# Kernel tuning notes

Hardware: AMD Instinct MI355X
Metric: run time of the kernel (lower is better)

Reference implementation:

```python
import jax, jax.numpy as jnp
import numpy as np

N_NODES = 100000
N_EDGES = 1200000
NFEAT, NHID, NCLASS = 64, 256, 40
DROP_RATE = 0.5
ORDER = 8


def setup_inputs() -> dict:
    key = jax.random.key(0)
    k = jax.random.split(key, 6)
    x = jax.random.normal(k[0], (N_NODES, NFEAT), dtype=jnp.float32)
    edge_index = jax.random.randint(k[1], (2, N_EDGES), 0, N_NODES, dtype=jnp.int64)
    stdv1 = 1.0 / np.sqrt(NHID)
    stdv2 = 1.0 / np.sqrt(NCLASS)
    W1 = jax.random.normal(k[2], (NFEAT, NHID), dtype=jnp.float32) * stdv1
    b1 = jax.random.normal(k[3], (NHID,), dtype=jnp.float32) * stdv1
    W2 = jax.random.normal(k[4], (NHID, NCLASS), dtype=jnp.float32) * stdv2
    b2 = jax.random.normal(k[5], (NCLASS,), dtype=jnp.float32) * stdv2
    return {"x": x, "edge_index": edge_index, "W1": W1, "b1": b1, "W2": W2, "b2": b2}


def _norm_adj(edge_index, n):
    # A + I, then D^{-1/2} (A+I) D^{-1/2}  (GCN symmetric normalization)
    loops = jnp.arange(n, dtype=edge_index.dtype)
    row = jnp.concatenate([edge_index[0], loops])
    col = jnp.concatenate([edge_index[1], loops])
    ones = jnp.ones(row.shape[0], dtype=jnp.float32)
    deg = jax.ops.segment_sum(ones, row, num_segments=n)  # row sums (self-loops guarantee deg>=1)
    d_inv_sqrt = 1.0 / jnp.sqrt(deg)
    ew = d_inv_sqrt[row] * d_inv_sqrt[col]  # [E+N] edge weights
    return row, col, ew


def reference(x, edge_index, W1, b1, W2, b2):
    n = x.shape[0]
    row, col, ew = _norm_adj(edge_index, n)

    def spmm(h):  # out[row] += ew * h[col]
        return jax.ops.segment_sum(ew[:, None] * h[col], row, num_segments=n)

    # eval-mode input scaling (training=False branch of GRAND.forward)
    h = x * (1.0 - DROP_RATE)
    y = h
    for _ in range(ORDER):
        h = spmm(h)
        y = y + h
    y = y / (ORDER + 1.0)

    # MLP in eval mode: dropouts are no-ops, use_bn=False
    hid = jax.nn.relu(y @ W1 + b1)
    return hid @ W2 + b2
```

## Files before the change

kernel.cpp:

```cpp
#include <hip/hip_runtime.h>

#define NN 100000
#define NE 1200000
#define NF 64
#define NH 256
#define NC 40
#define ORDER_C 8
#define SC 1024
#define BINB 1024
#define BCAP 165000
#define CCAP (NE + 7 * NN)

typedef __attribute__((ext_vector_type(8))) short short8;
typedef __attribute__((ext_vector_type(4))) float f32x4;

__device__ __forceinline__ unsigned bf16r(float x) {
    unsigned u = __float_as_uint(x);
    return (u + 0x7FFFu + ((u >> 16) & 1u)) >> 16;
}
__device__ __forceinline__ unsigned packbf(float lo, float hi) {
    return bf16r(lo) | (bf16r(hi) << 16);
}
__device__ __forceinline__ float bflo(unsigned u) { return __uint_as_float(u << 16); }
__device__ __forceinline__ float bfhi(unsigned u) { return __uint_as_float(u & 0xFFFF0000u); }


static __global__ __launch_bounds__(256) void k_bin(const int* __restrict__ rows,
                                                    const int* __restrict__ cols,
                                                    int* __restrict__ bcnt,
                                                    int* __restrict__ browb,
                                                    int* __restrict__ bcolb, int E)
{
    __shared__ int rbuf[BINB];
    __shared__ unsigned short lofs[BINB];
    __shared__ int hist[8], basew[8];
    int t = threadIdx.x;
    int e0 = blockIdx.x * BINB;
    int m = E - e0; if (m > BINB) m = BINB;
    if (t < 8) hist[t] = 0;
    __syncthreads();
    for (int i = t; i < m; i += 256) {
        int r = rows[e0 + i];
        rbuf[i] = r;
        int b = r / 12500;
        lofs[i] = (unsigned short)atomicAdd(&hist[b], 1);
    }
    __syncthreads();
    if (t < 8) basew[t] = atomicAdd(&bcnt[t], hist[t]);
    __syncthreads();
    for (int i = t; i < m; i += 256) {
        int r = rbuf[i];
        int b = r / 12500;
        size_t pos = (size_t)b * BCAP + basew[b] + lofs[i];
        browb[pos] = r;
        bcolb[pos] = cols[e0 + i];
    }
}


static __global__ __launch_bounds__(256) void k_cnt2(const int* __restrict__ browb,
                                                     const int* __restrict__ bcnt,
                                                     int* __restrict__ cnt)
{
    int grp = blockIdx.x & 7;
    int m = bcnt[grp];
    const int* src = browb + (size_t)grp * BCAP;
    int stride = (gridDim.x >> 3) * 256;
    for (int i = (blockIdx.x >> 3) * 256 + threadIdx.x; i < m; i += stride)
        atomicAdd(&cnt[src[i]], 1);
}


static __global__ __launch_bounds__(256) void k_bsum(const int* __restrict__ cnt,
                                                     int* __restrict__ bsum, int n)
{
    __shared__ int red[256];
    int t = threadIdx.x;
    int idx = blockIdx.x * SC + t * 4;
    int s = 0;
    if (idx + 3 < n) {
        int4 q = *(const int4*)&cnt[idx];
        s = ((q.x + 7) & ~7) + ((q.y + 7) & ~7) + ((q.z + 7) & ~7) + ((q.w + 7) & ~7);
    } else {
        for (int j = 0; j < 4; ++j) if (idx + j < n) s += (cnt[idx + j] + 7) & ~7;
    }
    red[t] = s;
    __syncthreads();
    for (int off = 128; off > 0; off >>= 1) {
        if (t < off) red[t] += red[t + off];
        __syncthreads();
    }
    if (t == 0) bsum[blockIdx.x] = red[0];
}

static __global__ __launch_bounds__(128) void k_scanb(const int* __restrict__ bsum,
                                                      int* __restrict__ boff,
                                                      int* __restrict__ rp, int nb, int n)
{
    __shared__ int red[128];
    int t = threadIdx.x;
    int v = (t < nb) ? bsum[t] : 0;
    red[t] = v;
    __syncthreads();
    for (int off = 1; off < 128; off <<= 1) {
        int x = (t >= off) ? red[t - off] : 0;
        __syncthreads();
        red[t] += x;
        __syncthreads();
    }
    if (t < nb) boff[t] = (t == 0) ? 0 : red[t - 1];
    if (t == 0) rp[n] = red[127];
}

static __global__ __launch_bounds__(256) void k_scan3(const int* __restrict__ cnt,
                                                      const int* __restrict__ boff,
                                                      int* __restrict__ rp,
                                                      float2* __restrict__ drd, int n)
{
    __shared__ int red[256];
    int t = threadIdx.x;
    int idx = blockIdx.x * SC + t * 4;
    int v[4] = {0, 0, 0, 0};
    if (idx + 3 < n) {
        int4 q = *(const int4*)&cnt[idx];
        v[0] = q.x; v[1] = q.y; v[2] = q.z; v[3] = q.w;
    } else {
        for (int j = 0; j < 4; ++j) if (idx + j < n) v[j] = cnt[idx + j];
    }
    int p[4];
    #pragma unroll
    for (int j = 0; j < 4; ++j) p[j] = (v[j] + 7) & ~7;
    red[t] = p[0] + p[1] + p[2] + p[3];
    __syncthreads();
    for (int off = 1; off < 256; off <<= 1) {
        int x = (t >= off) ? red[t - off] : 0;
        __syncthreads();
        red[t] += x;
        __syncthreads();
    }
    int run = ((t == 0) ? 0 : red[t - 1]) + boff[blockIdx.x];
    #pragma unroll
    for (int j = 0; j < 4; ++j) {
        if (idx + j < n) {
            rp[idx + j] = run;
            float d1 = rsqrtf((float)(v[j] + 1));
            drd[idx + j] = make_float2(d1, (float)(v[j] + 1) * d1);
            run += p[j];
        }
    }
}


static __global__ __launch_bounds__(256) void k_fillc(int4* __restrict__ ccol4, int cap4, int val)
{
    int i = blockIdx.x * 256 + threadIdx.x;
    if (i < cap4) ccol4[i] = make_int4(val, val, val, val);
}


static __global__ __launch_bounds__(256) void k_scat2(const int* __restrict__ browb,
                                                      const int* __restrict__ bcolb,
                                                      const int* __restrict__ bcnt,
                                                      int* __restrict__ fillpos,
                                                      int* __restrict__ ccol)
{
    int grp = blockIdx.x & 7;
    int m = bcnt[grp];
    const int* srcr = browb + (size_t)grp * BCAP;
    const int* srcc = bcolb + (size_t)grp * BCAP;
    int stride = (gridDim.x >> 3) * 256;
    for (int i = (blockIdx.x >> 3) * 256 + threadIdx.x; i < m; i += stride) {
        int r = srcr[i];
        int pos = atomicAdd(&fillpos[r], 1);
        ccol[pos] = srcc[i];
    }
}


static __global__ __launch_bounds__(256) void k_pack(const float* __restrict__ W1,
                                                     const float* __restrict__ W2,
                                                     unsigned short* __restrict__ w1f,
                                                     unsigned short* __restrict__ w2f)
{
    int t = blockIdx.x * 256 + threadIdx.x;
    if (t < 2048) {
        int lane = t & 63;
        int g = lane >> 4, col = (lane & 15) + ((t >> 6) & 15) * 16;
        int s = t >> 10;
        unsigned short* p = w1f + (size_t)t * 8;
        #pragma unroll
        for (int e = 0; e < 8; ++e) {
            int k = 32 * s + 8 * g + e;
            p[e] = (unsigned short)bf16r(W1[k * NH + col]);
        }
    } else if (t < 2048 + 1536) {
        int u = t - 2048;
        int lane = u & 63;
        int tile = u >> 6;
        int nt = tile % 3, s = tile / 3;
        int g = lane >> 4, col = (lane & 15) + nt * 16;
        unsigned short* p = w2f + (size_t)u * 8;
        #pragma unroll
        for (int e = 0; e < 8; ++e) {
            int k = 32 * s + 8 * g + e;
            p[e] = (col < NC) ? (unsigned short)bf16r(W2[k * NC + col]) : 0;
        }
    }
}


static __global__ __launch_bounds__(256) void k_init(const float4* __restrict__ x4,
                                                     float4* __restrict__ y4,
                                                     uint4* __restrict__ ga,
                                                     uint4* __restrict__ gbp,
                                                     const float2* __restrict__ drd,
                                                     int nchunk)
{
    int i = blockIdx.x * 256 + threadIdx.x;
    if (i >= nchunk) {
        if (i < nchunk + 8) {
            uint4 z = make_uint4(0, 0, 0, 0);
            ga[i] = z; gbp[i] = z;
        }
        return;
    }
    float d1 = drd[i >> 3].x;
    float4 a = x4[i * 2], b = x4[i * 2 + 1];
    a.x *= 0.5f; a.y *= 0.5f; a.z *= 0.5f; a.w *= 0.5f;
    b.x *= 0.5f; b.y *= 0.5f; b.z *= 0.5f; b.w *= 0.5f;
    y4[i * 2] = a; y4[i * 2 + 1] = b;
    ga[i] = make_uint4(packbf(a.x * d1, a.y * d1), packbf(a.z * d1, a.w * d1),
                       packbf(b.x * d1, b.y * d1), packbf(b.z * d1, b.w * d1));
}


template<bool ACC>
static __global__ __launch_bounds__(256) void k_spmm(const uint2* __restrict__ gb,
                                                     uint2* __restrict__ go,
                                                     float4* __restrict__ y4,
                                                     const int* __restrict__ rp,
                                                     const int* __restrict__ ccol,
                                                     const float2* __restrict__ drd, int n)
{
    int wid  = (blockIdx.x * 256 + threadIdx.x) >> 6;
    int lane = threadIdx.x & 63;
    int row  = wid * 4 + (lane >> 4);
    int j    = lane & 15;
    if (row >= n) return;
    int s = rp[row], e = rp[row + 1];

    float a0 = 0.f, a1 = 0.f, a2 = 0.f, a3 = 0.f;
    float b0 = 0.f, b1 = 0.f, b2 = 0.f, b3 = 0.f;
    for (int i = s; i < e; i += 8) {
        int4 cA = *(const int4*)&ccol[i];
        int4 cB = *(const int4*)&ccol[i + 4];
        uint2 h0 = gb[(size_t)cA.x * 16 + j];
        uint2 h1 = gb[(size_t)cA.y * 16 + j];
        uint2 h2 = gb[(size_t)cA.z * 16 + j];
        uint2 h3 = gb[(size_t)cA.w * 16 + j];
        uint2 h4 = gb[(size_t)cB.x * 16 + j];
        uint2 h5 = gb[(size_t)cB.y * 16 + j];
        uint2 h6 = gb[(size_t)cB.z * 16 + j];
        uint2 h7 = gb[(size_t)cB.w * 16 + j];
        a0 += bflo(h0.x); a1 += bfhi(h0.x); a2 += bflo(h0.y); a3 += bfhi(h0.y);
        b0 += bflo(h1.x); b1 += bfhi(h1.x); b2 += bflo(h1.y); b3 += bfhi(h1.y);
        a0 += bflo(h2.x); a1 += bfhi(h2.x); a2 += bflo(h2.y); a3 += bfhi(h2.y);
        b0 += bflo(h3.x); b1 += bfhi(h3.x); b2 += bflo(h3.y); b3 += bfhi(h3.y);
        a0 += bflo(h4.x); a1 += bfhi(h4.x); a2 += bflo(h4.y); a3 += bfhi(h4.y);
        b0 += bflo(h5.x); b1 += bfhi(h5.x); b2 += bflo(h5.y); b3 += bfhi(h5.y);
        a0 += bflo(h6.x); a1 += bfhi(h6.x); a2 += bflo(h6.y); a3 += bfhi(h6.y);
        b0 += bflo(h7.x); b1 += bfhi(h7.x); b2 += bflo(h7.y); b3 += bfhi(h7.y);
    }

    float2 dr = drd[row];
    uint2 gs = gb[(size_t)row * 16 + j];
    float g0 = bflo(gs.x), g1 = bfhi(gs.x), g2 = bflo(gs.y), g3 = bfhi(gs.y);
    float s0 = (a0 + b0) + g0;
    float s1 = (a1 + b1) + g1;
    float s2 = (a2 + b2) + g2;
    float s3 = (a3 + b3) + g3;
    float h0 = dr.x * s0, h1 = dr.x * s1, h2 = dr.x * s2, h3 = dr.x * s3;
    go[(size_t)row * 16 + j] = make_uint2(packbf(dr.x * h0, dr.x * h1),
                                          packbf(dr.x * h2, dr.x * h3));
    if (ACC) {
        float4 yv = y4[(size_t)row * 16 + j];
        yv.x += fmaf(g0, dr.y, h0);
        yv.y += fmaf(g1, dr.y, h1);
        yv.z += fmaf(g2, dr.y, h2);
        yv.w += fmaf(g3, dr.y, h3);
        y4[(size_t)row * 16 + j] = yv;
    }
}


#define YSTR 72
#define HSTR 264

static __global__ __launch_bounds__(256) void k_mlp(const float4* __restrict__ y4,
                                                    const short8* __restrict__ w1f,
                                                    const short8* __restrict__ w2f,
                                                    const float* __restrict__ b1,
                                                    const float* __restrict__ b2,
                                                    float* __restrict__ out, int n)
{
    __shared__ short lds[64 * HSTR];
    int t = threadIdx.x;
    int lane = t & 63;
    int w = t >> 6;
    int base = blockIdx.x * 64;
    const float S = 1.f / 9.f;

    {
        int r = t >> 2, q = t & 3;
        int row = base + r;
        unsigned v[8];
        if (row < n) {
            const float4* yp = y4 + (size_t)row * 16 + q * 4;
            #pragma unroll
            for (int i = 0; i < 4; ++i) {
                float4 f = yp[i];
                v[i * 2]     = packbf(f.x * S, f.y * S);
                v[i * 2 + 1] = packbf(f.z * S, f.w * S);
            }
        } else {
            #pragma unroll
            for (int i = 0; i < 8; ++i) v[i] = 0;
        }
        uint4* dst = (uint4*)&lds[r * YSTR + q * 16];
        dst[0] = make_uint4(v[0], v[1], v[2], v[3]);
        dst[1] = make_uint4(v[4], v[5], v[6], v[7]);
    }
    __syncthreads();

    int m = lane & 15, g = lane >> 4;

    f32x4 acc[4][4];
    {
        short8 a[4][2];
        #pragma unroll
        for (int mt = 0; mt < 4; ++mt)
            #pragma unroll
            for (int s = 0; s < 2; ++s)
                a[mt][s] = *(const short8*)&lds[(mt * 16 + m) * YSTR + s * 32 + g * 8];
        #pragma unroll
        for (int nt4 = 0; nt4 < 4; ++nt4) {
            int nt = w * 4 + nt4;
            short8 b0  = w1f[nt * 64 + lane];
            short8 b1v = w1f[(16 + nt) * 64 + lane];
            float bias = b1[nt * 16 + m];
            #pragma unroll
            for (int mt = 0; mt < 4; ++mt) {
                f32x4 c = {bias, bias, bias, bias};
                c = __builtin_amdgcn_mfma_f32_16x16x32_bf16(a[mt][0], b0,  c, 0, 0, 0);
                c = __builtin_amdgcn_mfma_f32_16x16x32_bf16(a[mt][1], b1v, c, 0, 0, 0);
                acc[mt][nt4] = c;
            }
        }
    }
    __syncthreads();

    {
        #pragma unroll
        for (int mt = 0; mt < 4; ++mt)
            #pragma unroll
            for (int nt4 = 0; nt4 < 4; ++nt4) {
                int col = w * 64 + nt4 * 16 + m;
                #pragma unroll
                for (int r = 0; r < 4; ++r) {
                    float hv = fmaxf(acc[mt][nt4][r], 0.f);
                    lds[(mt * 16 + g * 4 + r) * HSTR + col] = (short)bf16r(hv);
                }
            }
    }
    __syncthreads();

    {
        short8 a2[8];
        #pragma unroll
        for (int s = 0; s < 8; ++s)
            a2[s] = *(const short8*)&lds[(w * 16 + m) * HSTR + s * 32 + g * 8];
        #pragma unroll
        for (int nt = 0; nt < 3; ++nt) {
            int col = nt * 16 + m;
            float bias = (col < NC) ? b2[col] : 0.f;
            f32x4 c = {bias, bias, bias, bias};
            #pragma unroll
            for (int s = 0; s < 8; ++s)
                c = __builtin_amdgcn_mfma_f32_16x16x32_bf16(a2[s], w2f[(s * 3 + nt) * 64 + lane], c, 0, 0, 0);
            if (col < NC) {
                #pragma unroll
                for (int r = 0; r < 4; ++r) {
                    int row = base + w * 16 + g * 4 + r;
                    if (row < n) out[(size_t)row * NC + col] = c[r];
                }
            }
        }
    }
}


extern "C" void kernel_launch(void* const* d_in, const int* in_sizes, int n_in,
                              void* d_out, int out_size, void* d_ws, size_t ws_size,
                              hipStream_t stream)
{
    const float* x  = (const float*)d_in[0];
    const int*   ei = (const int*)d_in[1];
    const float* W1 = (const float*)d_in[2];
    const float* b1 = (const float*)d_in[3];
    const float* W2 = (const float*)d_in[4];
    const float* b2 = (const float*)d_in[5];
    float* out = (float*)d_out;

    const int n = NN, E = NE;
    const int nb = (n + SC - 1) / SC;

    char* ws = (char*)d_ws;
    size_t off = 0;
    auto alloc = [&](size_t bytes) -> void* {
        void* p = ws + off;
        off = (off + bytes + 255) & ~(size_t)255;
        return p;
    };
    int*    cnt   = (int*)   alloc((size_t)n * 4);
    int*    fill  = (int*)   alloc((size_t)n * 4);
    int*    rp    = (int*)   alloc((size_t)(n + 1) * 4);
    float2* drd   = (float2*)alloc((size_t)n * 8);
    int*    bsum  = (int*)   alloc(128 * 4);
    int*    boff  = (int*)   alloc(128 * 4);
    int*    bcnt  = (int*)   alloc(8 * 4);
    int*    browb = (int*)   alloc((size_t)8 * BCAP * 4);
    int*    bcolb = (int*)   alloc((size_t)8 * BCAP * 4);
    int*    ccol  = (int*)   alloc((size_t)CCAP * 4);
    unsigned short* w1f = (unsigned short*)alloc(2048 * 8 * 2);
    unsigned short* w2f = (unsigned short*)alloc(1536 * 8 * 2);
    uint4* ha   = (uint4*)alloc((size_t)(n + 1) * NF * 2);
    uint4* hbuf = (uint4*)alloc((size_t)(n + 1) * NF * 2);
    float* y    = (float*)alloc((size_t)n * NF * 4);

    hipMemsetAsync(cnt, 0, (size_t)n * 4, stream);
    hipMemsetAsync(bcnt, 0, 8 * 4, stream);

    const int* rows = ei;
    const int* cols = ei + E;

    k_bin   <<<(E + BINB - 1) / BINB, 256, 0, stream>>>(rows, cols, bcnt, browb, bcolb, E);
    k_cnt2  <<<4096, 256, 0, stream>>>(browb, bcnt, cnt);
    k_bsum  <<<nb, 256, 0, stream>>>(cnt, bsum, n);
    k_scanb <<<1, 128, 0, stream>>>(bsum, boff, rp, nb, n);
    k_scan3 <<<nb, 256, 0, stream>>>(cnt, boff, rp, drd, n);
    hipMemcpyAsync(fill, rp, (size_t)n * 4, hipMemcpyDeviceToDevice, stream);
    k_fillc <<<(CCAP / 4 + 255) / 256, 256, 0, stream>>>((int4*)ccol, CCAP / 4, n);
    k_scat2 <<<4096, 256, 0, stream>>>(browb, bcolb, bcnt, fill, ccol);
    k_pack  <<<14, 256, 0, stream>>>(W1, W2, w1f, w2f);

    int nchunk = n * 8;
    k_init<<<(nchunk + 8 + 255) / 256, 256, 0, stream>>>((const float4*)x, (float4*)y,
                                                         ha, hbuf, drd, nchunk);

    uint4* cur = ha;
    uint4* nxt = hbuf;
    int spmm_blocks = (n + 15) / 16;
    for (int it = 0; it < ORDER_C; ++it) {
        if (it & 1)
            k_spmm<true><<<spmm_blocks, 256, 0, stream>>>((const uint2*)cur, (uint2*)nxt,
                                                          (float4*)y, rp, ccol, drd, n);
        else
            k_spmm<false><<<spmm_blocks, 256, 0, stream>>>((const uint2*)cur, (uint2*)nxt,
                                                           (float4*)y, rp, ccol, drd, n);
        uint4* tswap = cur; cur = nxt; nxt = tswap;
    }

    k_mlp<<<(n + 63) / 64, 256, 0, stream>>>((const float4*)y, (const short8*)w1f,
                                             (const short8*)w2f, b1, b2, out, n);
}
```

Baseline: 405.9 us.

## Use XCD-aware dynamic chunk claiming for CSR build and drop fill pass

The count and scatter kernels now read the XCC id from a hardware register, start on the bin group matching their XCD, and claim work in 1024-edge chunks through per-group atomic counters instead of a static block-to-group mapping. The goal is better L2 locality and load balance across bins. The separate padding-fill kernel is removed, and padding slots are written inside the scan kernel instead. The final SpMM iteration also skips writing the unused next-hop buffer. In exchange, the change adds atomic claim traffic, extra syncthreads per chunk, and a dependence on the hardware-register read.

```diff
diff --git a/kernel.cpp b/kernel.cpp
--- a/kernel.cpp
+++ b/kernel.cpp
@@ -10,6 +10,7 @@
 #define BINB 1024
 #define BCAP 165000
 #define CCAP (NE + 7 * NN)
+#define CHUNK 1024
 
 typedef __attribute__((ext_vector_type(8))) short short8;
 typedef __attribute__((ext_vector_type(4))) float f32x4;
@@ -23,6 +24,12 @@
 }
 __device__ __forceinline__ float bflo(unsigned u) { return __uint_as_float(u << 16); }
 __device__ __forceinline__ float bfhi(unsigned u) { return __uint_as_float(u & 0xFFFF0000u); }
+
+__device__ __forceinline__ int xcd_id() {
+    unsigned xcc;
+    asm volatile("s_getreg_b32 %0, hwreg(HW_REG_XCC_ID)" : "=s"(xcc));
+    return (int)(xcc & 7u);
+}
 
 
 static __global__ __launch_bounds__(256) void k_bin(const int* __restrict__ rows,
@@ -60,14 +67,26 @@
 
 static __global__ __launch_bounds__(256) void k_cnt2(const int* __restrict__ browb,
                                                      const int* __restrict__ bcnt,
-                                                     int* __restrict__ cnt)
-{
-    int grp = blockIdx.x & 7;
-    int m = bcnt[grp];
-    const int* src = browb + (size_t)grp * BCAP;
-    int stride = (gridDim.x >> 3) * 256;
-    for (int i = (blockIdx.x >> 3) * 256 + threadIdx.x; i < m; i += stride)
-        atomicAdd(&cnt[src[i]], 1);
+                                                     int* __restrict__ cnt,
+                                                     int* __restrict__ claim)
+{
+    __shared__ int schunk;
+    int xcc = xcd_id();
+    for (int gg = 0; gg < 8; ++gg) {
+        int grp = (xcc + gg) & 7;
+        int m = bcnt[grp];
+        const int* src = browb + (size_t)grp * BCAP;
+        for (;;) {
+            __syncthreads();
+            if (threadIdx.x == 0) schunk = atomicAdd(&claim[grp], CHUNK);
+            __syncthreads();
+            int base = schunk;
+            if (base >= m) break;
+            int end = base + CHUNK; if (end > m) end = m;
+            for (int i = base + threadIdx.x; i < end; i += 256)
+                atomicAdd(&cnt[src[i]], 1);
+        }
+    }
 }
 
 
@@ -115,7 +134,8 @@
 static __global__ __launch_bounds__(256) void k_scan3(const int* __restrict__ cnt,
                                                       const int* __restrict__ boff,
                                                       int* __restrict__ rp,
-                                                      float2* __restrict__ drd, int n)
+                                                      float2* __restrict__ drd,
+                                                      int* __restrict__ ccol, int n)
 {
     __shared__ int red[256];
     int t = threadIdx.x;
@@ -145,16 +165,10 @@
             rp[idx + j] = run;
             float d1 = rsqrtf((float)(v[j] + 1));
             drd[idx + j] = make_float2(d1, (float)(v[j] + 1) * d1);
+            for (int q = v[j]; q < p[j]; ++q) ccol[run + q] = n;
             run += p[j];
         }
     }
-}
-
-
-static __global__ __launch_bounds__(256) void k_fillc(int4* __restrict__ ccol4, int cap4, int val)
-{
-    int i = blockIdx.x * 256 + threadIdx.x;
-    if (i < cap4) ccol4[i] = make_int4(val, val, val, val);
 }
 
 
@@ -162,17 +176,28 @@
                                                       const int* __restrict__ bcolb,
                                                       const int* __restrict__ bcnt,
                                                       int* __restrict__ fillpos,
-                                                      int* __restrict__ ccol)
-{
-    int grp = blockIdx.x & 7;
-    int m = bcnt[grp];
-    const int* srcr = browb + (size_t)grp * BCAP;
-    const int* srcc = bcolb + (size_t)grp * BCAP;
-    int stride = (gridDim.x >> 3) * 256;
-    for (int i = (blockIdx.x >> 3) * 256 + threadIdx.x; i < m; i += stride) {
-        int r = srcr[i];
-        int pos = atomicAdd(&fillpos[r], 1);
-        ccol[pos] = srcc[i];
+                                                      int* __restrict__ ccol,
+                                                      int* __restrict__ claim)
+{
+    __shared__ int schunk;
+    int xcc = xcd_id();
+    for (int gg = 0; gg < 8; ++gg) {
+        int grp = (xcc + gg) & 7;
+        int m = bcnt[grp];
+        const int* srcr = browb + (size_t)grp * BCAP;
+        const int* srcc = bcolb + (size_t)grp * BCAP;
+        for (;;) {
+            __syncthreads();
+            if (threadIdx.x == 0) schunk = atomicAdd(&claim[grp], CHUNK);
+            __syncthreads();
+            int base = schunk;
+            if (base >= m) break;
+            int end = base + CHUNK; if (end > m) end = m;
+            for (int i = base + threadIdx.x; i < end; i += 256) {
+                int pos = atomicAdd(&fillpos[srcr[i]], 1);
+                ccol[pos] = srcc[i];
+            }
+        }
     }
 }
 
@@ -234,7 +259,7 @@
 }
 
 
-template<bool ACC>
+template<bool ACC, bool WRITEG>
 static __global__ __launch_bounds__(256) void k_spmm(const uint2* __restrict__ gb,
                                                      uint2* __restrict__ go,
                                                      float4* __restrict__ y4,
@@ -280,8 +305,9 @@
     float s2 = (a2 + b2) + g2;
     float s3 = (a3 + b3) + g3;
     float h0 = dr.x * s0, h1 = dr.x * s1, h2 = dr.x * s2, h3 = dr.x * s3;
-    go[(size_t)row * 16 + j] = make_uint2(packbf(dr.x * h0, dr.x * h1),
-                                          packbf(dr.x * h2, dr.x * h3));
+    if (WRITEG)
+        go[(size_t)row * 16 + j] = make_uint2(packbf(dr.x * h0, dr.x * h1),
+                                              packbf(dr.x * h2, dr.x * h3));
     if (ACC) {
         float4 yv = y4[(size_t)row * 16 + j];
         yv.x += fmaf(g0, dr.y, h0);
@@ -421,16 +447,18 @@
         off = (off + bytes + 255) & ~(size_t)255;
         return p;
     };
-    int*    cnt   = (int*)   alloc((size_t)n * 4);
-    int*    fill  = (int*)   alloc((size_t)n * 4);
-    int*    rp    = (int*)   alloc((size_t)(n + 1) * 4);
-    float2* drd   = (float2*)alloc((size_t)n * 8);
-    int*    bsum  = (int*)   alloc(128 * 4);
-    int*    boff  = (int*)   alloc(128 * 4);
-    int*    bcnt  = (int*)   alloc(8 * 4);
-    int*    browb = (int*)   alloc((size_t)8 * BCAP * 4);
-    int*    bcolb = (int*)   alloc((size_t)8 * BCAP * 4);
-    int*    ccol  = (int*)   alloc((size_t)CCAP * 4);
+    int*    cnt    = (int*)   alloc((size_t)n * 4);
+    int*    fill   = (int*)   alloc((size_t)n * 4);
+    int*    rp     = (int*)   alloc((size_t)(n + 1) * 4);
+    float2* drd    = (float2*)alloc((size_t)n * 8);
+    int*    bsum   = (int*)   alloc(128 * 4);
+    int*    boff   = (int*)   alloc(128 * 4);
+    int*    bcnt   = (int*)   alloc(8 * 4);
+    int*    claimA = (int*)   alloc(8 * 4);
+    int*    claimB = (int*)   alloc(8 * 4);
+    int*    browb  = (int*)   alloc((size_t)8 * BCAP * 4);
+    int*    bcolb  = (int*)   alloc((size_t)8 * BCAP * 4);
+    int*    ccol   = (int*)   alloc((size_t)CCAP * 4);
     unsigned short* w1f = (unsigned short*)alloc(2048 * 8 * 2);
     unsigned short* w2f = (unsigned short*)alloc(1536 * 8 * 2);
     uint4* ha   = (uint4*)alloc((size_t)(n + 1) * NF * 2);
@@ -439,18 +467,19 @@
 
     hipMemsetAsync(cnt, 0, (size_t)n * 4, stream);
     hipMemsetAsync(bcnt, 0, 8 * 4, stream);
+    hipMemsetAsync(claimA, 0, 8 * 4, stream);
+    hipMemsetAsync(claimB, 0, 8 * 4, stream);
 
     const int* rows = ei;
     const int* cols = ei + E;
 
     k_bin   <<<(E + BINB - 1) / BINB, 256, 0, stream>>>(rows, cols, bcnt, browb, bcolb, E);
-    k_cnt2  <<<4096, 256, 0, stream>>>(browb, bcnt, cnt);
+    k_cnt2  <<<1024, 256, 0, stream>>>(browb, bcnt, cnt, claimA);
     k_bsum  <<<nb, 256, 0, stream>>>(cnt, bsum, n);
     k_scanb <<<1, 128, 0, stream>>>(bsum, boff, rp, nb, n);
-    k_scan3 <<<nb, 256, 0, stream>>>(cnt, boff, rp, drd, n);
+    k_scan3 <<<nb, 256, 0, stream>>>(cnt, boff, rp, drd, ccol, n);
     hipMemcpyAsync(fill, rp, (size_t)n * 4, hipMemcpyDeviceToDevice, stream);
-    k_fillc <<<(CCAP / 4 + 255) / 256, 256, 0, stream>>>((int4*)ccol, CCAP / 4, n);
-    k_scat2 <<<4096, 256, 0, stream>>>(browb, bcolb, bcnt, fill, ccol);
+    k_scat2 <<<1024, 256, 0, stream>>>(browb, bcolb, bcnt, fill, ccol, claimB);
     k_pack  <<<14, 256, 0, stream>>>(W1, W2, w1f, w2f);
 
     int nchunk = n * 8;
@@ -461,12 +490,17 @@
     uint4* nxt = hbuf;
     int spmm_blocks = (n + 15) / 16;
     for (int it = 0; it < ORDER_C; ++it) {
-        if (it & 1)
-            k_spmm<true><<<spmm_blocks, 256, 0, stream>>>((const uint2*)cur, (uint2*)nxt,
-                                                          (float4*)y, rp, ccol, drd, n);
+        bool acc = (it & 1) != 0;
+        bool wg  = (it != ORDER_C - 1);
+        if (acc && wg)
+            k_spmm<true, true><<<spmm_blocks, 256, 0, stream>>>((const uint2*)cur, (uint2*)nxt,
+                                                                (float4*)y, rp, ccol, drd, n);
+        else if (acc)
+            k_spmm<true, false><<<spmm_blocks, 256, 0, stream>>>((const uint2*)cur, (uint2*)nxt,
+                                                                 (float4*)y, rp, ccol, drd, n);
         else
-            k_spmm<false><<<spmm_blocks, 256, 0, stream>>>((const uint2*)cur, (uint2*)nxt,
-                                                           (float4*)y, rp, ccol, drd, n);
+            k_spmm<false, true><<<spmm_blocks, 256, 0, stream>>>((const uint2*)cur, (uint2*)nxt,
+                                                                 (float4*)y, rp, ccol, drd, n);
         uint4* tswap = cur; cur = nxt; nxt = tswap;
     }
 
```

After: 584.3 us. +44.0%, slower.
